# Optimization experiments

Measured on AMD Instinct MI355X. Metric: run time of the kernel, lower is better.

The kernel has to match this reference:

```python
import jax, jax.numpy as jnp
import numpy as np


def setup_inputs() -> dict:
    key = jax.random.key(0)
    k1, k2, k3, k4 = jax.random.split(key, 4)
    B, Tv, Ta, D = 8, 2048, 2048, 256
    return {
        "visual_features": jax.random.normal(k1, (B, Tv, D), dtype=jnp.float32),
        "audio_features": jax.random.normal(k2, (B, Ta, D), dtype=jnp.float32),
        "visual_weights": jax.random.uniform(k3, (D, D), dtype=jnp.float32),
        "audio_weights": jax.random.uniform(k4, (D, D), dtype=jnp.float32),
        "num_neighbors": 8,
    }


def _pairwise_l2(vm, am):
    # ||v - a|| via the expanded form to avoid the [B,Tv,Ta,D] intermediate.
    sq = (
        jnp.sum(vm * vm, -1)[:, :, None]
        + jnp.sum(am * am, -1)[:, None, :]
        - 2.0 * jnp.einsum("btd,bsd->bts", vm, am)
    )
    sq = jnp.maximum(sq, 0.0)
    # safe sqrt: subgradient 0 at 0 (matches torch.norm backward convention)
    return jnp.where(sq > 0, jnp.sqrt(jnp.where(sq > 0, sq, 1.0)), 0.0)


def reference(visual_features, audio_features, visual_weights, audio_weights, num_neighbors):
    vm = visual_features @ visual_weights  # [B,Tv,D]
    am = audio_features @ audio_weights    # [B,Ta,D]
    graph = jnp.exp(-_pairwise_l2(vm, am))  # [B,Tv,Ta]
    # topk over the visual axis (dim=1): move it last for lax.top_k
    _, idx = jax.lax.top_k(jnp.swapaxes(graph, 1, 2), num_neighbors)  # [B,Ta,k]
    idx = jnp.swapaxes(idx, 1, 2)  # [B,k,Ta]
    # broadcasted gather along axis 1: result [B,k,Ta,D]
    vn = jnp.take_along_axis(visual_features[:, :, None, :], idx[..., None], axis=1)
    an = jnp.take_along_axis(audio_features[:, :, None, :], idx[..., None], axis=1)
    # mean over dim=2 (the Ta axis of the gathered neighbors) -> [B,k,D]
    return vn.mean(axis=2), an.mean(axis=2)
```

## Files before the change

kernel.cpp:

```cpp
#include <hip/hip_runtime.h>
#include <cstddef>
#include <cstdint>

namespace {
constexpr int kB   = 8;
constexpr int kT   = 2048;
constexpr int kD   = 256;
constexpr int kK   = 8;
constexpr int kM   = kB * kT;
constexpr int kNCH = 64;
constexpr int kNC  = kB * kT;
constexpr int kColCap = 64;
constexpr int kOvCap  = 1 << 17;
constexpr int kStr = 264;
constexpr float kMinNormalF = 1.17549435e-38f;
}

typedef __attribute__((ext_vector_type(8)))  __bf16 bf16x8;
typedef __attribute__((ext_vector_type(16))) float  f32x16;

__device__ inline unsigned short f2bf_rne(float x) {
  unsigned u = __float_as_uint(x);
  unsigned r = (u + 0x7FFFu + ((u >> 16) & 1u)) >> 16;
  return (unsigned short)r;
}
__device__ inline float bf2f(unsigned short h) {
  return __uint_as_float((unsigned)h << 16);
}
union FragU { uint4 u4; bf16x8 v; };

__global__ __launch_bounds__(256) void transposeW2(const float* __restrict__ W0,
                                                   const float* __restrict__ W1,
                                                   unsigned short* __restrict__ T0,
                                                   unsigned short* __restrict__ T1) {
  const float* W = blockIdx.z ? W1 : W0;
  unsigned short* WT = blockIdx.z ? T1 : T0;
  __shared__ float tile[32][33];
  const int k0 = blockIdx.y * 32, c0 = blockIdx.x * 32;
  const int tx = threadIdx.x & 31, ty = threadIdx.x >> 5;
#pragma unroll
  for (int i = 0; i < 4; ++i)
    tile[ty + i * 8][tx] = W[(size_t)(k0 + ty + i * 8) * kD + c0 + tx];
  __syncthreads();
#pragma unroll
  for (int i = 0; i < 4; ++i)
    WT[(size_t)(c0 + ty + i * 8) * kD + k0 + tx] = f2bf_rne(tile[tx][ty + i * 8]);
}

__global__ __launch_bounds__(256) void gemm_areg(const float* __restrict__ Xv,
                                                 const float* __restrict__ Xa,
                                                 const unsigned short* __restrict__ WvT,
                                                 const unsigned short* __restrict__ WaT,
                                                 unsigned short* __restrict__ Cv,
                                                 unsigned short* __restrict__ Ca,
                                                 float* __restrict__ nv,
                                                 float* __restrict__ na) {
  __shared__ unsigned short Ws[64 * kStr];
  const int z = blockIdx.z;
  const float* X = z ? Xa : Xv;
  const unsigned short* WT = z ? WaT : WvT;
  unsigned short* Cb = z ? Ca : Cv;
  float* nrm = z ? na : nv;
  const int r0 = blockIdx.x * 128;
  const int c0 = blockIdx.y * 64;
  const int tid = threadIdx.x;
  const int w = tid >> 6, lane = tid & 63;
  const int half = lane >> 5, ln = lane & 31;

#pragma unroll
  for (int i = 0; i < 8; ++i) {
    const int idx = i * 256 + tid;
    const int row = idx >> 5, g = idx & 31;
    const uint4 v = *reinterpret_cast<const uint4*>(WT + (size_t)(c0 + row) * kD + g * 8);
    *reinterpret_cast<uint4*>(Ws + row * kStr + g * 8) = v;
  }
  const float* xrow = X + (size_t)(r0 + w * 32 + ln) * kD + half * 8;
  uint4 afr[16];
#pragma unroll
  for (int kc = 0; kc < 16; ++kc) {
    const float4 v0 = *reinterpret_cast<const float4*>(xrow + kc * 16);
    const float4 v1 = *reinterpret_cast<const float4*>(xrow + kc * 16 + 4);
    afr[kc].x = (unsigned)f2bf_rne(v0.x) | ((unsigned)f2bf_rne(v0.y) << 16);
    afr[kc].y = (unsigned)f2bf_rne(v0.z) | ((unsigned)f2bf_rne(v0.w) << 16);
    afr[kc].z = (unsigned)f2bf_rne(v1.x) | ((unsigned)f2bf_rne(v1.y) << 16);
    afr[kc].w = (unsigned)f2bf_rne(v1.z) | ((unsigned)f2bf_rne(v1.w) << 16);
  }
  f32x16 acc[2];
#pragma unroll
  for (int j = 0; j < 2; ++j)
#pragma unroll
    for (int i = 0; i < 16; ++i) acc[j][i] = 0.0f;
  __syncthreads();
#pragma unroll
  for (int kc = 0; kc < 16; ++kc) {
    FragU fa; fa.u4 = afr[kc];
#pragma unroll
    for (int cs = 0; cs < 2; ++cs) {
      FragU fb;
      fb.u4 = *reinterpret_cast<const uint4*>(Ws + (cs * 32 + ln) * kStr + kc * 16 + half * 8);
      acc[cs] = __builtin_amdgcn_mfma_f32_32x32x16_bf16(fa.v, fb.v, acc[cs], 0, 0, 0);
    }
  }
  float ns[16];
#pragma unroll
  for (int r = 0; r < 16; ++r) ns[r] = 0.0f;
#pragma unroll
  for (int cs = 0; cs < 2; ++cs) {
    const int col = c0 + cs * 32 + ln;
#pragma unroll
    for (int r = 0; r < 16; ++r) {
      const int row = r0 + w * 32 + (r & 3) + 8 * (r >> 2) + 4 * half;
      const unsigned short us = f2bf_rne(acc[cs][r]);
      Cb[(size_t)row * kD + col] = us;
      const float f = bf2f(us);
      ns[r] += f * f;
    }
  }
#pragma unroll
  for (int r = 0; r < 16; ++r) {
    float v = ns[r];
#pragma unroll
    for (int off = 1; off < 32; off <<= 1) v += __shfl_xor(v, off, 64);
    if (ln == 0) {
      const int row = r0 + w * 32 + (r & 3) + 8 * (r >> 2) + 4 * half;
      atomicAdd(nrm + row, v);
    }
  }
}

__global__ __launch_bounds__(256) void keys_areg(const unsigned short* __restrict__ vmb,
                                                 const unsigned short* __restrict__ amb,
                                                 const float* __restrict__ vn2,
                                                 const float* __restrict__ an2,
                                                 unsigned* __restrict__ colCount,
                                                 uint2* __restrict__ colRecs,
                                                 unsigned* __restrict__ ovCount,
                                                 uint2* __restrict__ ovRecs) {
  __shared__ unsigned short amS[64 * kStr];
  const int b = blockIdx.z;
  const int t0 = blockIdx.x * 128;
  const int sr0 = blockIdx.y * 128;
  const int tid = threadIdx.x;
  const int w = tid >> 6, lane = tid & 63;
  const int half = lane >> 5, ln = lane & 31;

  const unsigned short* arow = vmb + ((size_t)b * kT + t0 + w * 32 + ln) * kD + half * 8;
  uint4 afr[16];
#pragma unroll
  for (int kc = 0; kc < 16; ++kc)
    afr[kc] = *reinterpret_cast<const uint4*>(arow + kc * 16);

  const float* v2p = vn2 + (size_t)b * kT + t0 + w * 32;

  for (int st = 0; st < 2; ++st) {
    const int s0 = sr0 + st * 64;
    if (st) __syncthreads();
#pragma unroll
    for (int i = 0; i < 8; ++i) {
      const int idx = i * 256 + tid;
      const int row = idx >> 5, g = idx & 31;
      const uint4 v = *reinterpret_cast<const uint4*>(amb + ((size_t)b * kT + s0 + row) * kD + g * 8);
      *reinterpret_cast<uint4*>(amS + row * kStr + g * 8) = v;
    }
    f32x16 acc[2];
#pragma unroll
    for (int j = 0; j < 2; ++j)
#pragma unroll
      for (int i = 0; i < 16; ++i) acc[j][i] = 0.0f;
    __syncthreads();
#pragma unroll
    for (int kc = 0; kc < 16; ++kc) {
      FragU fa; fa.u4 = afr[kc];
#pragma unroll
      for (int ss = 0; ss < 2; ++ss) {
        FragU fb;
        fb.u4 = *reinterpret_cast<const uint4*>(amS + (ss * 32 + ln) * kStr + kc * 16 + half * 8);
        acc[ss] = __builtin_amdgcn_mfma_f32_32x32x16_bf16(fa.v, fb.v, acc[ss], 0, 0, 0);
      }
    }
#pragma unroll
    for (int ss = 0; ss < 2; ++ss) {
      const int s = s0 + ss * 32 + ln;
      const float a2 = an2[(size_t)b * kT + s];
      const int c = (b << 11) | s;
#pragma unroll
      for (int g = 0; g < 4; ++g) {
        const float4 v2 = *reinterpret_cast<const float4*>(v2p + g * 8 + half * 4);
        const float v2a[4] = {v2.x, v2.y, v2.z, v2.w};
#pragma unroll
        for (int q = 0; q < 4; ++q) {
          const float raw = v2a[q] + a2 - 2.0f * acc[ss][4 * g + q];
          if (raw < 7744.0f) {
            const float dist = sqrtf(fmaxf(raw, 0.0f));
            const float e = expf(-dist);
            if (e >= kMinNormalF) {
              const int t = t0 + w * 32 + g * 8 + half * 4 + q;
              const unsigned slot = atomicAdd(&colCount[c], 1u);
              if (slot < (unsigned)kColCap) {
                colRecs[(size_t)c * kColCap + slot] = make_uint2(__float_as_uint(e), (unsigned)t);
              } else {
                const unsigned pos = ((unsigned)b << 22) | ((unsigned)s << 11) | (unsigned)t;
                const unsigned oi = atomicAdd(ovCount, 1u);
                if (oi < (unsigned)kOvCap) ovRecs[oi] = make_uint2(__float_as_uint(e), pos);
              }
            }
          }
        }
      }
    }
  }
}

__global__ __launch_bounds__(256) void finalize_topk(const unsigned* __restrict__ colCount,
                                                     const uint2* __restrict__ colRecs,
                                                     const unsigned* __restrict__ ovCount,
                                                     const uint2* __restrict__ ovRecs,
                                                     int* __restrict__ idxT) {
  const int c = blockIdx.x * 256 + threadIdx.x;
  unsigned K[8];
  int T[8];
#pragma unroll
  for (int i = 0; i < 8; ++i) { K[i] = 0u; T[i] = 0x7FFFFFFF; }
  const int cnt = (int)colCount[c];
  const int m = min(cnt, kColCap);
  for (int i = 0; i < m; ++i) {
    const uint2 r = colRecs[(size_t)c * kColCap + i];
    const unsigned kx = r.x;
    const int tx = (int)r.y;
    if (kx > K[7] || (kx == K[7] && tx < T[7])) {
      K[7] = kx; T[7] = tx;
#pragma unroll
      for (int q = 7; q >= 1; --q) {
        const bool sw = (K[q] > K[q - 1]) || (K[q] == K[q - 1] && T[q] < T[q - 1]);
        if (sw) {
          const unsigned tk = K[q]; K[q] = K[q - 1]; K[q - 1] = tk;
          const int tt = T[q];      T[q] = T[q - 1]; T[q - 1] = tt;
        }
      }
    }
  }
  if (cnt > kColCap) {
    int n = (int)*ovCount;
    if (n > kOvCap) n = kOvCap;
    for (int i = 0; i < n; ++i) {
      const uint2 r = ovRecs[i];
      if ((int)(r.y >> 11) == c) {
        const unsigned kx = r.x;
        const int tx = (int)(r.y & 2047u);
        if (kx > K[7] || (kx == K[7] && tx < T[7])) {
          K[7] = kx; T[7] = tx;
#pragma unroll
          for (int q = 7; q >= 1; --q) {
            const bool sw = (K[q] > K[q - 1]) || (K[q] == K[q - 1] && T[q] < T[q - 1]);
            if (sw) {
              const unsigned tk = K[q]; K[q] = K[q - 1]; K[q - 1] = tk;
              const int tt = T[q];      T[q] = T[q - 1]; T[q - 1] = tt;
            }
          }
        }
      }
    }
  }
  int mcnt = 0;
#pragma unroll
  for (int i = 0; i < 8; ++i) if (K[i] > 0u) mcnt++;
  int outv[8];
#pragma unroll
  for (int i = 0; i < 8; ++i) outv[i] = T[i];
  int cand = 0;
  for (int r = mcnt; r < 8; ++r) {
    bool taken = true;
    while (taken) {
      taken = false;
#pragma unroll
      for (int q = 0; q < 8; ++q)
        if (q < mcnt && T[q] == cand) taken = true;
      if (taken) cand++;
    }
    outv[r] = cand++;
  }
  const int b = c >> 11, s = c & 2047;
#pragma unroll
  for (int r = 0; r < 8; ++r) idxT[((size_t)b * kK + r) * kT + s] = outv[r];
}

__global__ __launch_bounds__(256) void gather_kernel(const float* __restrict__ visual,
                                                     const float* __restrict__ audio,
                                                     const int* __restrict__ idxT,
                                                     float* __restrict__ pv,
                                                     float* __restrict__ pa) {
  const int blk = blockIdx.x;
  const int ch = blk & (kNCH - 1);
  const int bj = blk / kNCH;
  const int b = bj >> 3;
  const int d = threadIdx.x;
  const int* ip = idxT + (size_t)bj * kT + ch * (kT / kNCH);
  float accV = 0.f, accA = 0.f;
  for (int g = 0; g < kT / kNCH / 4; ++g) {
    const int4 cur = *reinterpret_cast<const int4*>(ip + g * 4);
    const int ts[4] = {cur.x, cur.y, cur.z, cur.w};
#pragma unroll
    for (int u = 0; u < 4; ++u) {
      const size_t base = ((size_t)b * kT + ts[u]) * kD + d;
      accV += visual[base];
      accA += audio[base];
    }
  }
  pv[(size_t)blk * kD + d] = accV;
  pa[(size_t)blk * kD + d] = accA;
}

__global__ __launch_bounds__(256) void reduce_kernel(const float* __restrict__ pv,
                                                     const float* __restrict__ pa,
                                                     float* __restrict__ out) {
  const int bj = blockIdx.x;
  const int d = threadIdx.x;
  float sV = 0.f, sA = 0.f;
#pragma unroll 8
  for (int ch = 0; ch < kNCH; ++ch) {
    sV += pv[((size_t)bj * kNCH + ch) * kD + d];
    sA += pa[((size_t)bj * kNCH + ch) * kD + d];
  }
  out[(size_t)bj * kD + d] = sV * (1.0f / kT);
  out[(size_t)kB * kK * kD + (size_t)bj * kD + d] = sA * (1.0f / kT);
}

extern "C" void kernel_launch(void* const* d_in, const int* in_sizes, int n_in,
                              void* d_out, int out_size, void* d_ws, size_t ws_size,
                              hipStream_t stream) {
  (void)in_sizes; (void)n_in; (void)out_size; (void)ws_size;
  const float* visual = (const float*)d_in[0];
  const float* audio  = (const float*)d_in[1];
  const float* Wv     = (const float*)d_in[2];
  const float* Wa     = (const float*)d_in[3];
  float* out = (float*)d_out;

  char* ws = (char*)d_ws;
  unsigned short* WvT = (unsigned short*)ws;
  unsigned short* WaT = WvT + (size_t)kD * kD;
  unsigned short* vmb = WaT + (size_t)kD * kD;
  unsigned short* amb = vmb + (size_t)kM * kD;
  float* vn2 = (float*)(amb + (size_t)kM * kD);
  float* an2 = vn2 + kM;
  unsigned* colCount = (unsigned*)(an2 + kM);
  unsigned* ovCount  = colCount + kNC;
  uint2* colRecs = (uint2*)(ovCount + 4);
  uint2* ovRecs  = colRecs + (size_t)kNC * kColCap;
  int* idxT = (int*)(ovRecs + kOvCap);
  float* pv = (float*)(idxT + (size_t)kB * kK * kT);
  float* pa = pv + (size_t)kB * kK * kNCH * kD;

  hipMemsetAsync(vn2, 0, (size_t)(2 * kM + kNC + 4) * sizeof(float), stream);
  transposeW2<<<dim3(kD / 32, kD / 32, 2), 256, 0, stream>>>(Wv, Wa, WvT, WaT);
  gemm_areg<<<dim3(kM / 128, kD / 64, 2), 256, 0, stream>>>(visual, audio, WvT, WaT,
                                                            vmb, amb, vn2, an2);
  keys_areg<<<dim3(kT / 128, kT / 128, kB), 256, 0, stream>>>(vmb, amb, vn2, an2,
                                                              colCount, colRecs, ovCount, ovRecs);
  finalize_topk<<<dim3(kNC / 256), 256, 0, stream>>>(colCount, colRecs, ovCount, ovRecs, idxT);
  gather_kernel<<<dim3(kB * kK * kNCH), 256, 0, stream>>>(visual, audio, idxT, pv, pa);
  reduce_kernel<<<dim3(kB * kK), 256, 0, stream>>>(pv, pa, out);
}
```

Measured before the change: 173.8 us.

## Restructure projection GEMM and distance kernel into 2x2 warp tiles via LDS

The projection GEMM now gives each block a 64-row strip across all 256 output columns. X is converted to bf16 once and staged through LDS, and the kernel loops over four W column tiles. This avoids re-reading and re-converting the fp32 input once per column tile. The distance/key kernel uses 64-row visual tiles with a 2x2 warp layout, so each warp computes one 32x32 MFMA tile and loads its A fragments from LDS instead of global memory. This lowers per-warp register pressure (one accumulator instead of two) and increases block count, at the cost of more LDS barriers and re-reading audio tiles for twice as many blocks.

```diff
diff --git a/kernel.cpp b/kernel.cpp
--- a/kernel.cpp
+++ b/kernel.cpp
@@ -47,162 +47,163 @@
     WT[(size_t)(c0 + ty + i * 8) * kD + k0 + tx] = f2bf_rne(tile[tx][ty + i * 8]);
 }
 
-__global__ __launch_bounds__(256) void gemm_areg(const float* __restrict__ Xv,
-                                                 const float* __restrict__ Xa,
-                                                 const unsigned short* __restrict__ WvT,
-                                                 const unsigned short* __restrict__ WaT,
-                                                 unsigned short* __restrict__ Cv,
-                                                 unsigned short* __restrict__ Ca,
-                                                 float* __restrict__ nv,
-                                                 float* __restrict__ na) {
-  __shared__ unsigned short Ws[64 * kStr];
-  const int z = blockIdx.z;
+__global__ __launch_bounds__(256) void gemm_hyb(const float* __restrict__ Xv,
+                                                const float* __restrict__ Xa,
+                                                const unsigned short* __restrict__ WvT,
+                                                const unsigned short* __restrict__ WaT,
+                                                unsigned short* __restrict__ Cv,
+                                                unsigned short* __restrict__ Ca,
+                                                float* __restrict__ nv,
+                                                float* __restrict__ na) {
+  __shared__ unsigned short S[64 * kStr];
+  const int z = blockIdx.y;
   const float* X = z ? Xa : Xv;
   const unsigned short* WT = z ? WaT : WvT;
   unsigned short* Cb = z ? Ca : Cv;
   float* nrm = z ? na : nv;
-  const int r0 = blockIdx.x * 128;
-  const int c0 = blockIdx.y * 64;
+  const int r0 = blockIdx.x * 64;
   const int tid = threadIdx.x;
   const int w = tid >> 6, lane = tid & 63;
+  const int wt = w & 1, wc = w >> 1;
+  const int half = lane >> 5, ln = lane & 31;
+
+#pragma unroll
+  for (int i = 0; i < 16; ++i) {
+    const int idx = i * 256 + tid;
+    const int row = idx >> 6, g = idx & 63;
+    const float4 v = *reinterpret_cast<const float4*>(X + (size_t)(r0 + row) * kD + g * 4);
+    ushort4 o;
+    o.x = f2bf_rne(v.x); o.y = f2bf_rne(v.y); o.z = f2bf_rne(v.z); o.w = f2bf_rne(v.w);
+    *reinterpret_cast<ushort4*>(S + row * kStr + g * 4) = o;
+  }
+  __syncthreads();
+  uint4 afr[16];
+#pragma unroll
+  for (int kc = 0; kc < 16; ++kc)
+    afr[kc] = *reinterpret_cast<const uint4*>(S + (wt * 32 + ln) * kStr + kc * 16 + half * 8);
+
+  float ns[16];
+#pragma unroll
+  for (int r = 0; r < 16; ++r) ns[r] = 0.0f;
+
+  for (int ct = 0; ct < 4; ++ct) {
+    const int c0 = ct * 64;
+    __syncthreads();
+#pragma unroll
+    for (int i = 0; i < 8; ++i) {
+      const int idx = i * 256 + tid;
+      const int row = idx >> 5, g = idx & 31;
+      const uint4 v = *reinterpret_cast<const uint4*>(WT + (size_t)(c0 + row) * kD + g * 8);
+      *reinterpret_cast<uint4*>(S + row * kStr + g * 8) = v;
+    }
+    __syncthreads();
+    f32x16 acc;
+#pragma unroll
+    for (int i = 0; i < 16; ++i) acc[i] = 0.0f;
+#pragma unroll
+    for (int kc = 0; kc < 16; ++kc) {
+      FragU fa, fb;
+      fa.u4 = afr[kc];
+      fb.u4 = *reinterpret_cast<const uint4*>(S + (wc * 32 + ln) * kStr + kc * 16 + half * 8);
+      acc = __builtin_amdgcn_mfma_f32_32x32x16_bf16(fa.v, fb.v, acc, 0, 0, 0);
+    }
+    const int col = c0 + wc * 32 + ln;
+#pragma unroll
+    for (int r = 0; r < 16; ++r) {
+      const int row = r0 + wt * 32 + (r & 3) + 8 * (r >> 2) + 4 * half;
+      const unsigned short us = f2bf_rne(acc[r]);
+      Cb[(size_t)row * kD + col] = us;
+      const float f = bf2f(us);
+      ns[r] += f * f;
+    }
+  }
+#pragma unroll
+  for (int r = 0; r < 16; ++r) {
+    float v = ns[r];
+#pragma unroll
+    for (int off = 1; off < 32; off <<= 1) v += __shfl_xor(v, off, 64);
+    if (ln == 0) {
+      const int row = r0 + wt * 32 + (r & 3) + 8 * (r >> 2) + 4 * half;
+      atomicAdd(nrm + row, v);
+    }
+  }
+}
+
+__global__ __launch_bounds__(256) void keys_hyb(const unsigned short* __restrict__ vmb,
+                                                const unsigned short* __restrict__ amb,
+                                                const float* __restrict__ vn2,
+                                                const float* __restrict__ an2,
+                                                unsigned* __restrict__ colCount,
+                                                uint2* __restrict__ colRecs,
+                                                unsigned* __restrict__ ovCount,
+                                                uint2* __restrict__ ovRecs) {
+  __shared__ unsigned short S[64 * kStr];
+  const int b = blockIdx.z;
+  const int t0 = blockIdx.x * 64;
+  const int sr0 = blockIdx.y * 128;
+  const int tid = threadIdx.x;
+  const int w = tid >> 6, lane = tid & 63;
+  const int wt = w & 1, wsc = w >> 1;
   const int half = lane >> 5, ln = lane & 31;
 
 #pragma unroll
   for (int i = 0; i < 8; ++i) {
     const int idx = i * 256 + tid;
     const int row = idx >> 5, g = idx & 31;
-    const uint4 v = *reinterpret_cast<const uint4*>(WT + (size_t)(c0 + row) * kD + g * 8);
-    *reinterpret_cast<uint4*>(Ws + row * kStr + g * 8) = v;
-  }
-  const float* xrow = X + (size_t)(r0 + w * 32 + ln) * kD + half * 8;
+    const uint4 v = *reinterpret_cast<const uint4*>(vmb + ((size_t)b * kT + t0 + row) * kD + g * 8);
+    *reinterpret_cast<uint4*>(S + row * kStr + g * 8) = v;
+  }
+  __syncthreads();
   uint4 afr[16];
 #pragma unroll
-  for (int kc = 0; kc < 16; ++kc) {
-    const float4 v0 = *reinterpret_cast<const float4*>(xrow + kc * 16);
-    const float4 v1 = *reinterpret_cast<const float4*>(xrow + kc * 16 + 4);
-    afr[kc].x = (unsigned)f2bf_rne(v0.x) | ((unsigned)f2bf_rne(v0.y) << 16);
-    afr[kc].y = (unsigned)f2bf_rne(v0.z) | ((unsigned)f2bf_rne(v0.w) << 16);
-    afr[kc].z = (unsigned)f2bf_rne(v1.x) | ((unsigned)f2bf_rne(v1.y) << 16);
-    afr[kc].w = (unsigned)f2bf_rne(v1.z) | ((unsigned)f2bf_rne(v1.w) << 16);
-  }
-  f32x16 acc[2];
-#pragma unroll
-  for (int j = 0; j < 2; ++j)
-#pragma unroll
-    for (int i = 0; i < 16; ++i) acc[j][i] = 0.0f;
-  __syncthreads();
-#pragma unroll
-  for (int kc = 0; kc < 16; ++kc) {
-    FragU fa; fa.u4 = afr[kc];
-#pragma unroll
-    for (int cs = 0; cs < 2; ++cs) {
-      FragU fb;
-      fb.u4 = *reinterpret_cast<const uint4*>(Ws + (cs * 32 + ln) * kStr + kc * 16 + half * 8);
-      acc[cs] = __builtin_amdgcn_mfma_f32_32x32x16_bf16(fa.v, fb.v, acc[cs], 0, 0, 0);
-    }
-  }
-  float ns[16];
-#pragma unroll
-  for (int r = 0; r < 16; ++r) ns[r] = 0.0f;
-#pragma unroll
-  for (int cs = 0; cs < 2; ++cs) {
-    const int col = c0 + cs * 32 + ln;
-#pragma unroll
-    for (int r = 0; r < 16; ++r) {
-      const int row = r0 + w * 32 + (r & 3) + 8 * (r >> 2) + 4 * half;
-      const unsigned short us = f2bf_rne(acc[cs][r]);
-      Cb[(size_t)row * kD + col] = us;
-      const float f = bf2f(us);
-      ns[r] += f * f;
-    }
-  }
-#pragma unroll
-  for (int r = 0; r < 16; ++r) {
-    float v = ns[r];
-#pragma unroll
-    for (int off = 1; off < 32; off <<= 1) v += __shfl_xor(v, off, 64);
-    if (ln == 0) {
-      const int row = r0 + w * 32 + (r & 3) + 8 * (r >> 2) + 4 * half;
-      atomicAdd(nrm + row, v);
-    }
-  }
-}
-
-__global__ __launch_bounds__(256) void keys_areg(const unsigned short* __restrict__ vmb,
-                                                 const unsigned short* __restrict__ amb,
-                                                 const float* __restrict__ vn2,
-                                                 const float* __restrict__ an2,
-                                                 unsigned* __restrict__ colCount,
-                                                 uint2* __restrict__ colRecs,
-                                                 unsigned* __restrict__ ovCount,
-                                                 uint2* __restrict__ ovRecs) {
-  __shared__ unsigned short amS[64 * kStr];
-  const int b = blockIdx.z;
-  const int t0 = blockIdx.x * 128;
-  const int sr0 = blockIdx.y * 128;
-  const int tid = threadIdx.x;
-  const int w = tid >> 6, lane = tid & 63;
-  const int half = lane >> 5, ln = lane & 31;
-
-  const unsigned short* arow = vmb + ((size_t)b * kT + t0 + w * 32 + ln) * kD + half * 8;
-  uint4 afr[16];
-#pragma unroll
   for (int kc = 0; kc < 16; ++kc)
-    afr[kc] = *reinterpret_cast<const uint4*>(arow + kc * 16);
-
-  const float* v2p = vn2 + (size_t)b * kT + t0 + w * 32;
+    afr[kc] = *reinterpret_cast<const uint4*>(S + (wt * 32 + ln) * kStr + kc * 16 + half * 8);
+
+  const float* v2p = vn2 + (size_t)b * kT + t0 + wt * 32;
 
   for (int st = 0; st < 2; ++st) {
     const int s0 = sr0 + st * 64;
-    if (st) __syncthreads();
+    __syncthreads();
 #pragma unroll
     for (int i = 0; i < 8; ++i) {
       const int idx = i * 256 + tid;
       const int row = idx >> 5, g = idx & 31;
       const uint4 v = *reinterpret_cast<const uint4*>(amb + ((size_t)b * kT + s0 + row) * kD + g * 8);
-      *reinterpret_cast<uint4*>(amS + row * kStr + g * 8) = v;
-    }
-    f32x16 acc[2];
-#pragma unroll
-    for (int j = 0; j < 2; ++j)
-#pragma unroll
-      for (int i = 0; i < 16; ++i) acc[j][i] = 0.0f;
+      *reinterpret_cast<uint4*>(S + row * kStr + g * 8) = v;
+    }
     __syncthreads();
+    f32x16 acc;
+#pragma unroll
+    for (int i = 0; i < 16; ++i) acc[i] = 0.0f;
 #pragma unroll
     for (int kc = 0; kc < 16; ++kc) {
-      FragU fa; fa.u4 = afr[kc];
-#pragma unroll
-      for (int ss = 0; ss < 2; ++ss) {
-        FragU fb;
-        fb.u4 = *reinterpret_cast<const uint4*>(amS + (ss * 32 + ln) * kStr + kc * 16 + half * 8);
-        acc[ss] = __builtin_amdgcn_mfma_f32_32x32x16_bf16(fa.v, fb.v, acc[ss], 0, 0, 0);
-      }
-    }
-#pragma unroll
-    for (int ss = 0; ss < 2; ++ss) {
-      const int s = s0 + ss * 32 + ln;
-      const float a2 = an2[(size_t)b * kT + s];
-      const int c = (b << 11) | s;
-#pragma unroll
-      for (int g = 0; g < 4; ++g) {
-        const float4 v2 = *reinterpret_cast<const float4*>(v2p + g * 8 + half * 4);
-        const float v2a[4] = {v2.x, v2.y, v2.z, v2.w};
-#pragma unroll
-        for (int q = 0; q < 4; ++q) {
-          const float raw = v2a[q] + a2 - 2.0f * acc[ss][4 * g + q];
-          if (raw < 7744.0f) {
-            const float dist = sqrtf(fmaxf(raw, 0.0f));
-            const float e = expf(-dist);
-            if (e >= kMinNormalF) {
-              const int t = t0 + w * 32 + g * 8 + half * 4 + q;
-              const unsigned slot = atomicAdd(&colCount[c], 1u);
-              if (slot < (unsigned)kColCap) {
-                colRecs[(size_t)c * kColCap + slot] = make_uint2(__float_as_uint(e), (unsigned)t);
-              } else {
-                const unsigned pos = ((unsigned)b << 22) | ((unsigned)s << 11) | (unsigned)t;
-                const unsigned oi = atomicAdd(ovCount, 1u);
-                if (oi < (unsigned)kOvCap) ovRecs[oi] = make_uint2(__float_as_uint(e), pos);
-              }
+      FragU fa, fb;
+      fa.u4 = afr[kc];
+      fb.u4 = *reinterpret_cast<const uint4*>(S + (wsc * 32 + ln) * kStr + kc * 16 + half * 8);
+      acc = __builtin_amdgcn_mfma_f32_32x32x16_bf16(fa.v, fb.v, acc, 0, 0, 0);
+    }
+    const int s = s0 + wsc * 32 + ln;
+    const float a2 = an2[(size_t)b * kT + s];
+    const int c = (b << 11) | s;
+#pragma unroll
+    for (int g = 0; g < 4; ++g) {
+      const float4 v2 = *reinterpret_cast<const float4*>(v2p + g * 8 + half * 4);
+      const float v2a[4] = {v2.x, v2.y, v2.z, v2.w};
+#pragma unroll
+      for (int q = 0; q < 4; ++q) {
+        const float raw = v2a[q] + a2 - 2.0f * acc[4 * g + q];
+        if (raw < 7744.0f) {
+          const float dist = sqrtf(fmaxf(raw, 0.0f));
+          const float e = expf(-dist);
+          if (e >= kMinNormalF) {
+            const int t = t0 + wt * 32 + g * 8 + half * 4 + q;
+            const unsigned slot = atomicAdd(&colCount[c], 1u);
+            if (slot < (unsigned)kColCap) {
+              colRecs[(size_t)c * kColCap + slot] = make_uint2(__float_as_uint(e), (unsigned)t);
+            } else {
+              const unsigned pos = ((unsigned)b << 22) | ((unsigned)s << 11) | (unsigned)t;
+              const unsigned oi = atomicAdd(ovCount, 1u);
+              if (oi < (unsigned)kOvCap) ovRecs[oi] = make_uint2(__float_as_uint(e), pos);
             }
           }
         }
@@ -352,10 +353,10 @@
 
   hipMemsetAsync(vn2, 0, (size_t)(2 * kM + kNC + 4) * sizeof(float), stream);
   transposeW2<<<dim3(kD / 32, kD / 32, 2), 256, 0, stream>>>(Wv, Wa, WvT, WaT);
-  gemm_areg<<<dim3(kM / 128, kD / 64, 2), 256, 0, stream>>>(visual, audio, WvT, WaT,
-                                                            vmb, amb, vn2, an2);
-  keys_areg<<<dim3(kT / 128, kT / 128, kB), 256, 0, stream>>>(vmb, amb, vn2, an2,
-                                                              colCount, colRecs, ovCount, ovRecs);
+  gemm_hyb<<<dim3(kM / 64, 2), 256, 0, stream>>>(visual, audio, WvT, WaT,
+                                                 vmb, amb, vn2, an2);
+  keys_hyb<<<dim3(kT / 64, kT / 128, kB), 256, 0, stream>>>(vmb, amb, vn2, an2,
+                                                            colCount, colRecs, ovCount, ovRecs);
   finalize_topk<<<dim3(kNC / 256), 256, 0, stream>>>(colCount, colRecs, ovCount, ovRecs, idxT);
   gather_kernel<<<dim3(kB * kK * kNCH), 256, 0, stream>>>(visual, audio, idxT, pv, pa);
   reduce_kernel<<<dim3(kB * kK), 256, 0, stream>>>(pv, pa, out);
```

Result: slower. 179.4 us (+3.2%).
